# Optimization experiments

Measured on AMD Instinct MI355X. Metric: run time of the kernel, lower is better.

The kernel has to match this reference:

```python
import jax, jax.numpy as jnp
import numpy as np

D_MODEL = 512
H = 8
DEPTH = D_MODEL // H
TOPK = 16
TAU_HID = max(4, D_MODEL // 2)  # 256
TAU_EPS = 1e-6
DT = 1.0
T_SCALAR = 1.0  # default t in call()


def setup_inputs() -> dict:
    key = jax.random.key(0)
    ks = jax.random.split(key, 24)
    B, T = 2, 1024
    D2 = 2 * DEPTH

    def w(k, shape, fan_in):
        return jax.random.normal(k, shape, dtype=jnp.float32) / np.sqrt(fan_in)

    inp = {
        "x": jax.random.normal(ks[0], (B, T, D_MODEL), dtype=jnp.float32),
        "Wq": w(ks[1], (D_MODEL, D_MODEL), D_MODEL), "bq": jnp.zeros((D_MODEL,), jnp.float32),
        "Wk": w(ks[2], (D_MODEL, D_MODEL), D_MODEL), "bk": jnp.zeros((D_MODEL,), jnp.float32),
        "Wv": w(ks[3], (D_MODEL, D_MODEL), D_MODEL), "bv": jnp.zeros((D_MODEL,), jnp.float32),
        "Wo": w(ks[4], (D_MODEL, D_MODEL), D_MODEL), "bo": jnp.zeros((D_MODEL,), jnp.float32),
        "Wpi": w(ks[5], (D2, D_MODEL), D2), "bpi": jnp.zeros((D_MODEL,), jnp.float32),
        "Wpo": w(ks[6], (D_MODEL, 1), D_MODEL), "bpo": jnp.zeros((1,), jnp.float32),
        "Wta": w(ks[7], (D2, 1), D2), "bta": jnp.zeros((1,), jnp.float32),
        "Wtb": w(ks[8], (D2, 1), D2), "btb": jnp.zeros((1,), jnp.float32),
        "Wti": w(ks[9], (D2, TAU_HID), D2), "bti": jnp.zeros((TAU_HID,), jnp.float32),
        "Wto": w(ks[10], (TAU_HID, 1), TAU_HID), "bto": jnp.zeros((1,), jnp.float32),
    }
    return inp


def reference(x, Wq, bq, Wk, bk, Wv, bv, Wo, bo,
              Wpi, bpi, Wpo, bpo, Wta, bta, Wtb, btb, Wti, bti, Wto, bto):
    B, T, _ = x.shape

    def split_heads(z):
        return z.reshape(B, T, H, DEPTH).transpose(0, 2, 1, 3)  # [B,H,T,D]

    qh = split_heads(x @ Wq + bq)
    kh = split_heads(x @ Wk + bk)
    vh = split_heads(x @ Wv + bv)

    # top-k pairwise scores (q @ k^T), select K keys per query
    scores = jnp.einsum('bhqd,bhkd->bhqk', qh, kh)  # [B,H,T,T]
    _, idx = jax.lax.top_k(scores, TOPK)            # [B,H,T,K]

    # gather k and v at top-k indices -> [B,H,T,K,D]
    kg = jnp.take_along_axis(kh[:, :, None, :, :], idx[..., None], axis=3)
    vg = jnp.take_along_axis(vh[:, :, None, :, :], idx[..., None], axis=3)

    # per-pair features [q_i ; k_j] -> [B,H,T,K,2D]
    qt = jnp.broadcast_to(qh[:, :, :, None, :], (B, H, T, TOPK, DEPTH))
    pairs = jnp.concatenate([qt, kg], axis=-1)

    # phi: Dense(d_model) -> Dense(1) -> sigmoid
    phi = jax.nn.sigmoid(((pairs @ Wpi + bpi) @ Wpo + bpo)[..., 0])
    # time interpolation: sigmoid(a*t + b)
    t_a = (pairs @ Wta + bta)[..., 0]
    t_b = (pairs @ Wtb + btb)[..., 0]
    t_interp = jax.nn.sigmoid(t_a * T_SCALAR + t_b)
    # tau: Dense(d_model//2) -> Dense(1) -> softplus + eps
    tau = jax.nn.softplus(((pairs @ Wti + bti) @ Wto + bto)[..., 0]) + TAU_EPS

    # mode == 'exact'
    attn_logits = phi / tau * (1.0 - jnp.exp(-tau * t_interp))
    attn = jax.nn.softmax(attn_logits, axis=-1)  # [B,H,T,K]

    out_h = jnp.einsum('bhqk,bhqkd->bhqd', attn, vg) * DT  # [B,H,T,D]
    combined = out_h.transpose(0, 2, 1, 3).reshape(B, T, D_MODEL)
    return combined @ Wo + bo  # return_sequences=True
```

## Files before the change

### kernel.cpp

```cpp
#include <hip/hip_runtime.h>
#include <math.h>

#define BDIM 2
#define TT 1024
#define NH 8
#define HD 64
#define NTOPK 16
#define NBH 16
#define NTOK 16384

__global__ __launch_bounds__(256) void k_collapse64(
    const float* __restrict__ Wpi, const float* __restrict__ bpi,
    const float* __restrict__ Wpo, const float* __restrict__ bpo,
    const float* __restrict__ Wti, const float* __restrict__ bti,
    const float* __restrict__ Wto, const float* __restrict__ bto,
    double* __restrict__ wphid, double* __restrict__ wtaud,
    double* __restrict__ ccd) {
  int tid = threadIdx.x;
  int blk = blockIdx.x;
  if (blk < 16) {
    int r = blk * 16 + (tid >> 4);
    int l = tid & 15;
    double s = 0.;
    if (r < 128) {
      for (int i = 0; i < 32; ++i)
        s += (double)Wpi[r * 512 + l + 16 * i] * (double)Wpo[l + 16 * i];
    } else {
      int rr = r - 128;
      for (int i = 0; i < 16; ++i)
        s += (double)Wti[rr * 256 + l + 16 * i] * (double)Wto[l + 16 * i];
    }
#pragma unroll
    for (int off = 8; off >= 1; off >>= 1) s += __shfl_xor(s, off, 64);
    if (l == 0) {
      if (r < 128) wphid[r] = s;
      else wtaud[r - 128] = s;
    }
  } else {
    int lane = tid & 63;
    if (tid < 64) {
      double p = 0.;
      for (int c = lane; c < 512; c += 64) p += (double)bpi[c] * (double)Wpo[c];
#pragma unroll
      for (int off = 32; off >= 1; off >>= 1) p += __shfl_xor(p, off, 64);
      if (lane == 0) ccd[0] = p + (double)bpo[0];
    } else if (tid < 128) {
      double p = 0.;
      for (int c = lane; c < 256; c += 64) p += (double)bti[c] * (double)Wto[c];
#pragma unroll
      for (int off = 32; off >= 1; off >>= 1) p += __shfl_xor(p, off, 64);
      if (lane == 0) ccd[1] = p + (double)bto[0];
    }
  }
}

__device__ __forceinline__ void gemm_body(
    const float* __restrict__ A, const float* __restrict__ W,
    const float* __restrict__ bias, float* __restrict__ out,
    int bm, int bn, int mode) {
  __shared__ float As[32][68];
  __shared__ float Bs[32][64];
  const int tid = threadIdx.x;
  const int tx = tid & 15;
  const int ty = tid >> 4;
  float acc[4][4] = {{0.f, 0.f, 0.f, 0.f}};
  for (int k0 = 0; k0 < 512; k0 += 32) {
#pragma unroll
    for (int i = 0; i < 2; ++i) {
      int idx = i * 256 + tid;
      int row = idx >> 3;
      int c4 = (idx & 7) << 2;
      float4 av = *(const float4*)&A[(bm + row) * 512 + k0 + c4];
      As[c4 + 0][row] = av.x;
      As[c4 + 1][row] = av.y;
      As[c4 + 2][row] = av.z;
      As[c4 + 3][row] = av.w;
    }
#pragma unroll
    for (int i = 0; i < 2; ++i) {
      int idx = i * 256 + tid;
      int br = idx >> 4;
      int bc = (idx & 15) << 2;
      *(float4*)&Bs[br][bc] = *(const float4*)&W[(k0 + br) * 512 + bn + bc];
    }
    __syncthreads();
#pragma unroll
    for (int kk = 0; kk < 32; ++kk) {
      float4 a = *(const float4*)&As[kk][ty * 4];
      float4 b = *(const float4*)&Bs[kk][tx << 2];
      acc[0][0] = fmaf(a.x, b.x, acc[0][0]);
      acc[0][1] = fmaf(a.x, b.y, acc[0][1]);
      acc[0][2] = fmaf(a.x, b.z, acc[0][2]);
      acc[0][3] = fmaf(a.x, b.w, acc[0][3]);
      acc[1][0] = fmaf(a.y, b.x, acc[1][0]);
      acc[1][1] = fmaf(a.y, b.y, acc[1][1]);
      acc[1][2] = fmaf(a.y, b.z, acc[1][2]);
      acc[1][3] = fmaf(a.y, b.w, acc[1][3]);
      acc[2][0] = fmaf(a.z, b.x, acc[2][0]);
      acc[2][1] = fmaf(a.z, b.y, acc[2][1]);
      acc[2][2] = fmaf(a.z, b.z, acc[2][2]);
      acc[2][3] = fmaf(a.z, b.w, acc[2][3]);
      acc[3][0] = fmaf(a.w, b.x, acc[3][0]);
      acc[3][1] = fmaf(a.w, b.y, acc[3][1]);
      acc[3][2] = fmaf(a.w, b.z, acc[3][2]);
      acc[3][3] = fmaf(a.w, b.w, acc[3][3]);
    }
    __syncthreads();
  }
#pragma unroll
  for (int i = 0; i < 4; ++i) {
    int row = bm + ty * 4 + i;
    float4 r;
    r.x = acc[i][0] + bias[bn + tx * 4 + 0];
    r.y = acc[i][1] + bias[bn + tx * 4 + 1];
    r.z = acc[i][2] + bias[bn + tx * 4 + 2];
    r.w = acc[i][3] + bias[bn + tx * 4 + 3];
    if (mode == 0) {
      *(float4*)&out[row * 512 + bn + tx * 4] = r;
    } else {
      int bb = row >> 10;
      int tt2 = row & 1023;
      int head = bn >> 6;
      *(float4*)&out[(((bb * NH + head) * TT + tt2) << 6) + tx * 4] = r;
    }
  }
}

__global__ __launch_bounds__(256) void k_gemm(
    const float* __restrict__ A, const float* __restrict__ W,
    const float* __restrict__ bias, float* __restrict__ out, int mode) {
  gemm_body(A, W, bias, out, blockIdx.y * 64, blockIdx.x * 64, mode);
}

__global__ __launch_bounds__(256) void k_gemm_qkv(
    const float* __restrict__ A,
    const float* __restrict__ Wq, const float* __restrict__ bq,
    const float* __restrict__ Wk, const float* __restrict__ bk,
    const float* __restrict__ Wv, const float* __restrict__ bv,
    float* __restrict__ Qf, float* __restrict__ Kf, float* __restrict__ Vf) {
  int which = blockIdx.x >> 3;
  int bn = (blockIdx.x & 7) * 64;
  const float* W = (which == 0) ? Wq : (which == 1) ? Wk : Wv;
  const float* b = (which == 0) ? bq : (which == 1) ? bk : bv;
  float* out = (which == 0) ? Qf : (which == 1) ? Kf : Vf;
  gemm_body(A, W, b, out, blockIdx.y * 64, bn, 1);
}

__global__ __launch_bounds__(256) void k_tokscal64(
    const float* __restrict__ Qg, const float* __restrict__ Kg,
    const double* __restrict__ wphid, const float* __restrict__ Wta,
    const float* __restrict__ Wtb, const double* __restrict__ wtaud,
    double4* __restrict__ sqd4, double4* __restrict__ skd4) {
  __shared__ double wp[128], wa[128], wb[128], wt[128];
  int tid = threadIdx.x;
  if (tid < 128) {
    wp[tid] = wphid[tid];
    wa[tid] = (double)Wta[tid];
    wb[tid] = (double)Wtb[tid];
    wt[tid] = wtaud[tid];
  }
  __syncthreads();
  int tok = blockIdx.x * 256 + tid;
  const float* qr = Qg + (size_t)tok * 64;
  const float* kr = Kg + (size_t)tok * 64;
  double sp = 0., sa = 0., sb = 0., st = 0.;
  double kp = 0., ka = 0., kb2 = 0., kt = 0.;
#pragma unroll
  for (int d = 0; d < 64; ++d) {
    double q = (double)qr[d];
    double k = (double)kr[d];
    sp += q * wp[d];
    sa += q * wa[d];
    sb += q * wb[d];
    st += q * wt[d];
    kp += k * wp[64 + d];
    ka += k * wa[64 + d];
    kb2 += k * wb[64 + d];
    kt += k * wt[64 + d];
  }
  sqd4[tok] = make_double4(sp, sa, sb, st);
  skd4[tok] = make_double4(kp, ka, kb2, kt);
}

__global__ __launch_bounds__(256) void k_score(
    const float* __restrict__ Qf, const float* __restrict__ Kf,
    float* __restrict__ Sc) {
  __shared__ float As[32][132];
  __shared__ float Bs[32][132];
  const int bn = blockIdx.x * 128;
  const int bm = blockIdx.y * 128;
  const int bh = blockIdx.z;
  const float* A = Qf + (size_t)bh * (TT * 64);
  const float* K = Kf + (size_t)bh * (TT * 64);
  float* out = Sc + (size_t)bh * (TT * 1024);
  const int tid = threadIdx.x;
  const int tx = tid & 15;
  const int ty = tid >> 4;
  float acc[8][8];
#pragma unroll
  for (int i = 0; i < 8; ++i)
#pragma unroll
    for (int j = 0; j < 8; ++j) acc[i][j] = 0.f;
  for (int k0 = 0; k0 < 64; k0 += 32) {
#pragma unroll
    for (int i = 0; i < 4; ++i) {
      int idx = i * 256 + tid;
      int row = idx >> 3;
      int c4 = (idx & 7) << 2;
      float4 av = *(const float4*)&A[(size_t)(bm + row) * 64 + k0 + c4];
      As[c4 + 0][row] = av.x;
      As[c4 + 1][row] = av.y;
      As[c4 + 2][row] = av.z;
      As[c4 + 3][row] = av.w;
      float4 kv = *(const float4*)&K[(size_t)(bn + row) * 64 + k0 + c4];
      Bs[c4 + 0][row] = kv.x;
      Bs[c4 + 1][row] = kv.y;
      Bs[c4 + 2][row] = kv.z;
      Bs[c4 + 3][row] = kv.w;
    }
    __syncthreads();
#pragma unroll
    for (int kk = 0; kk < 32; ++kk) {
      float4 alo = *(const float4*)&As[kk][ty * 8];
      float4 ahi = *(const float4*)&As[kk][ty * 8 + 4];
      float4 blo = *(const float4*)&Bs[kk][tx * 8];
      float4 bhi = *(const float4*)&Bs[kk][tx * 8 + 4];
      float a[8] = {alo.x, alo.y, alo.z, alo.w, ahi.x, ahi.y, ahi.z, ahi.w};
      float b[8] = {blo.x, blo.y, blo.z, blo.w, bhi.x, bhi.y, bhi.z, bhi.w};
#pragma unroll
      for (int i = 0; i < 8; ++i)
#pragma unroll
        for (int j = 0; j < 8; ++j)
          acc[i][j] = fmaf(a[i], b[j], acc[i][j]);
    }
    __syncthreads();
  }
#pragma unroll
  for (int i = 0; i < 8; ++i) {
    float4 r0 = make_float4(acc[i][0], acc[i][1], acc[i][2], acc[i][3]);
    float4 r1 = make_float4(acc[i][4], acc[i][5], acc[i][6], acc[i][7]);
    size_t base = (size_t)(bm + ty * 8 + i) * 1024 + bn + tx * 8;
    *(float4*)&out[base] = r0;
    *(float4*)&out[base + 4] = r1;
  }
}

__global__ __launch_bounds__(256) void k_topk(
    const float* __restrict__ Sc, const float* __restrict__ Vg,
    const double4* __restrict__ sqd4, const double4* __restrict__ skd4,
    const double* __restrict__ ccd, const float* __restrict__ btaP,
    const float* __restrict__ btbP, float* __restrict__ C) {
  const int tid = threadIdx.x;
  const int lane = tid & 63;
  const int wv = tid >> 6;
  const int qg = blockIdx.x * 4 + wv;
  const int bh = qg >> 10;
  const int qa = qg & 1023;
  const int bb = bh >> 3;
  const int hh = bh & 7;
  const float* rowp = Sc + (size_t)qg * 1024;
  const float* Vbh = Vg + (size_t)bh * (TT * 64);

  float v[16];
#pragma unroll
  for (int g = 0; g < 4; ++g) {
    float4 t = *(const float4*)&rowp[g * 256 + lane * 4];
    v[g * 4 + 0] = t.x;
    v[g * 4 + 1] = t.y;
    v[g * 4 + 2] = t.z;
    v[g * 4 + 3] = t.w;
  }
  float gv[4];
  int gi[4];
  const int lbase = lane << 2;
#pragma unroll
  for (int g = 0; g < 4; ++g) {
    float nv = v[4 * g];
    int ne = 0;
#pragma unroll
    for (int e = 1; e < 4; ++e) {
      if (v[4 * g + e] > nv) { nv = v[4 * g + e]; ne = e; }
    }
    gv[g] = nv;
    gi[g] = (g << 8) | lbase | ne;
  }
  int myk = 0;
#pragma unroll 1
  for (int it = 0; it < NTOPK; ++it) {
    float cv = gv[0];
    int ci = gi[0];
#pragma unroll
    for (int g = 1; g < 4; ++g) {
      if (gv[g] > cv) { cv = gv[g]; ci = gi[g]; }
    }
    float M = cv;
#pragma unroll
    for (int off = 32; off >= 1; off >>= 1)
      M = fmaxf(M, __shfl_xor(M, off, 64));
    unsigned long long tied = __ballot(cv == M);
    int J;
    if (__popcll(tied) == 1) {
      int src = __ffsll(tied) - 1;
      J = __builtin_amdgcn_readfirstlane(__shfl(ci, src, 64));
    } else {
      int cj = (cv == M) ? ci : 0x7FFFFFFF;
#pragma unroll
      for (int off = 32; off >= 1; off >>= 1) {
        int oj = __shfl_xor(cj, off, 64);
        cj = (oj < cj) ? oj : cj;
      }
      J = __builtin_amdgcn_readfirstlane(cj);
    }
    if (lane == it) myk = J;
    const int owner = (J >> 2) & 63;
    const int g2 = J >> 8;
    const int e2 = J & 3;
    const bool isown = (lane == owner);
#pragma unroll
    for (int g = 0; g < 4; ++g) {
      if (g == g2) {
#pragma unroll
        for (int e = 0; e < 4; ++e) {
          if (e == e2) {
            v[4 * g + e] = isown ? -INFINITY : v[4 * g + e];
          }
        }
        float nv = v[4 * g];
        int ne = 0;
#pragma unroll
        for (int e = 1; e < 4; ++e) {
          if (v[4 * g + e] > nv) { nv = v[4 * g + e]; ne = e; }
        }
        gv[g] = nv;
        gi[g] = (g << 8) | lbase | ne;
      }
    }
  }
  const double cphi = ccd[0];
  const double ctau = ccd[1];
  const double bta0 = (double)btaP[0];
  const double btb0 = (double)btbP[0];
  double4 sq = sqd4[qg];
  float logit = -INFINITY;
  if (lane < 16) {
    double4 sk = skd4[bh * TT + myk];
    float xs = (float)(sq.x + sk.x + cphi);
    float ta = (float)(sq.y + sk.y + bta0);
    float tb = (float)(sq.z + sk.z + btb0);
    float tl = (float)(sq.w + sk.w + ctau);
    float phi = 1.f / (1.f + __expf(-xs));
    float ti = 1.f / (1.f + __expf(-(ta + tb)));
    float tau = fmaxf(tl, 0.f) + log1pf(__expf(-fabsf(tl))) + 1e-6f;
    logit = phi / tau * (1.f - __expf(-tau * ti));
  }
  float m = logit;
#pragma unroll
  for (int off = 8; off >= 1; off >>= 1) m = fmaxf(m, __shfl_xor(m, off, 64));
  float e = (lane < 16) ? __expf(logit - m) : 0.f;
  float ssum = e;
#pragma unroll
  for (int off = 8; off >= 1; off >>= 1) ssum += __shfl_xor(ssum, off, 64);
  float w = e / ssum;
  float outv = 0.f;
#pragma unroll
  for (int k2 = 0; k2 < NTOPK; ++k2) {
    float wk = __shfl(w, k2, 64);
    int ik = __shfl(myk, k2, 64);
    outv = fmaf(wk, Vbh[(size_t)ik * 64 + lane], outv);
  }
  C[(bb * TT + qa) * 512 + hh * 64 + lane] = outv;
}

__global__ __launch_bounds__(256) void k_attn(
    const float* __restrict__ Qg, const float* __restrict__ Kg,
    const float* __restrict__ Vg, const double4* __restrict__ sqd4,
    const double4* __restrict__ skd4, const double* __restrict__ ccd,
    const float* __restrict__ btaP, const float* __restrict__ btbP,
    float* __restrict__ C) {
  __shared__ float qs[8][64];
  __shared__ float sc[8][1024];
  const int bh = blockIdx.y;
  const int q0 = blockIdx.x * 8;
  const int tid = threadIdx.x;
  const int lane = tid & 63;
  const int wv = tid >> 6;
  if (tid < 128) {
    int q = tid >> 4, d4 = (tid & 15) << 2;
    *(float4*)&qs[q][d4] = *(const float4*)&Qg[(size_t)(bh * TT + q0 + q) * 64 + d4];
  }
  __syncthreads();
#pragma unroll 1
  for (int c = 0; c < 4; ++c) {
    const int kb = (c * 4 + wv) * 64;
    const float* krow = &Kg[(size_t)(bh * TT + kb + lane) * 64];
    float4 kr[16];
#pragma unroll
    for (int i = 0; i < 16; ++i) kr[i] = *(const float4*)&krow[i * 4];
#pragma unroll
    for (int q = 0; q < 8; ++q) {
      float s = 0.f;
#pragma unroll
      for (int i = 0; i < 16; ++i) {
        float4 q4 = *(const float4*)&qs[q][i * 4];
        s = fmaf(q4.x, kr[i].x, s);
        s = fmaf(q4.y, kr[i].y, s);
        s = fmaf(q4.z, kr[i].z, s);
        s = fmaf(q4.w, kr[i].w, s);
      }
      sc[q][kb + lane] = s;
    }
  }
  __syncthreads();
  const double cphi = ccd[0];
  const double ctau = ccd[1];
  const double bta0 = (double)btaP[0];
  const double btb0 = (double)btbP[0];
  const int bb = bh >> 3;
  const int hh = bh & 7;
  const float* Vbh = Vg + (size_t)bh * (TT * 64);
#pragma unroll 1
  for (int qq = 0; qq < 2; ++qq) {
    const int ql = wv * 2 + qq;
    const int qa = q0 + ql;
    const float* rowp = &sc[ql][0];
    float v[16];
#pragma unroll
    for (int jj = 0; jj < 16; ++jj) v[jj] = rowp[jj * 64 + lane];
    float gv[4];
    int gj[4];
#pragma unroll
    for (int g = 0; g < 4; ++g) {
      gv[g] = v[4 * g];
      gj[g] = 4 * g;
#pragma unroll
      for (int e = 1; e < 4; ++e) {
        if (v[4 * g + e] > gv[g]) { gv[g] = v[4 * g + e]; gj[g] = 4 * g + e; }
      }
    }
    int myk = 0;
#pragma unroll 1
    for (int it = 0; it < NTOPK; ++it) {
      float bvv = gv[0];
      int bjj = gj[0];
#pragma unroll
      for (int g = 1; g < 4; ++g) {
        if (gv[g] > bvv) { bvv = gv[g]; bjj = gj[g]; }
      }
      int bj = bjj * 64 + lane;
#pragma unroll
      for (int off = 32; off >= 1; off >>= 1) {
        float ov = __shfl_xor(bvv, off, 64);
        int oj = __shfl_xor(bj, off, 64);
        if (ov > bvv || (ov == bvv && oj < bj)) { bvv = ov; bj = oj; }
      }
      if (lane == it) myk = bj;
      int owner = bj & 63;
      int slot = bj >> 6;
      if (lane == owner) {
#pragma unroll
        for (int jj = 0; jj < 16; ++jj)
          if (jj == slot) v[jj] = -INFINITY;
        int g2 = slot >> 2;
#pragma unroll
        for (int g = 0; g < 4; ++g) {
          if (g == g2) {
            float ngv = v[4 * g];
            int ngj = 4 * g;
#pragma unroll
            for (int e = 1; e < 4; ++e) {
              if (v[4 * g + e] > ngv) { ngv = v[4 * g + e]; ngj = 4 * g + e; }
            }
            gv[g] = ngv;
            gj[g] = ngj;
          }
        }
      }
    }
    double4 sq = sqd4[bh * TT + qa];
    double logit = -INFINITY;
    if (lane < 16) {
      double4 sk = skd4[bh * TT + myk];
      double phi = 1.0 / (1.0 + exp(-(sq.x + sk.x + cphi)));
      double ta = sq.y + sk.y + bta0;
      double tb = sq.z + sk.z + btb0;
      double ti = 1.0 / (1.0 + exp(-(ta * 1.0 + tb)));
      double tl = sq.w + sk.w + ctau;
      double tau = fmax(tl, 0.0) + log1p(exp(-fabs(tl))) + 1e-6;
      logit = phi / tau * (1.0 - exp(-tau * ti));
    }
    double m = logit;
#pragma unroll
    for (int off = 8; off >= 1; off >>= 1) {
      double om = __shfl_xor(m, off, 64);
      m = fmax(m, om);
    }
    double e = (lane < 16) ? exp(logit - m) : 0.0;
    double ssum = e;
#pragma unroll
    for (int off = 8; off >= 1; off >>= 1) ssum += __shfl_xor(ssum, off, 64);
    double w = e / ssum;
    double outv = 0.0;
#pragma unroll
    for (int k2 = 0; k2 < NTOPK; ++k2) {
      double wk = __shfl(w, k2, 64);
      int ik = __shfl(myk, k2, 64);
      outv += wk * (double)Vbh[(size_t)ik * 64 + lane];
    }
    C[(bb * TT + qa) * 512 + hh * 64 + lane] = (float)outv;
  }
}

extern "C" void kernel_launch(void* const* d_in, const int* in_sizes, int n_in,
                              void* d_out, int out_size, void* d_ws, size_t ws_size,
                              hipStream_t stream) {
  (void)in_sizes; (void)n_in; (void)out_size;
  const float* x   = (const float*)d_in[0];
  const float* Wq  = (const float*)d_in[1];
  const float* bq  = (const float*)d_in[2];
  const float* Wk  = (const float*)d_in[3];
  const float* bk  = (const float*)d_in[4];
  const float* Wv  = (const float*)d_in[5];
  const float* bv  = (const float*)d_in[6];
  const float* Wo  = (const float*)d_in[7];
  const float* bo  = (const float*)d_in[8];
  const float* Wpi = (const float*)d_in[9];
  const float* bpi = (const float*)d_in[10];
  const float* Wpo = (const float*)d_in[11];
  const float* bpo = (const float*)d_in[12];
  const float* Wta = (const float*)d_in[13];
  const float* bta = (const float*)d_in[14];
  const float* Wtb = (const float*)d_in[15];
  const float* btb = (const float*)d_in[16];
  const float* Wti = (const float*)d_in[17];
  const float* bti = (const float*)d_in[18];
  const float* Wto = (const float*)d_in[19];
  const float* bto = (const float*)d_in[20];

  double* wsd = (double*)d_ws;
  double4* sqd4 = (double4*)wsd;
  double4* skd4 = (double4*)(wsd + 65536);
  double* wphid = wsd + 131072;
  double* wtaud = wsd + 131200;
  double* ccd   = wsd + 131328;
  float* fs = (float*)(wsd + 131332);
  float* Qf = fs;
  float* Kf = fs + 1048576;
  float* Vf = fs + 2097152;
  float* Cf = fs + 3145728;
  float* Sc = fs + 4194304;
  const size_t need = (size_t)131332 * 8 + (size_t)(4194304 + 16777216) * 4;

  hipLaunchKernelGGL(k_collapse64, dim3(17), dim3(256), 0, stream,
                     Wpi, bpi, Wpo, bpo, Wti, bti, Wto, bto, wphid, wtaud, ccd);
  hipLaunchKernelGGL(k_gemm_qkv, dim3(24, 32), dim3(256), 0, stream,
                     x, Wq, bq, Wk, bk, Wv, bv, Qf, Kf, Vf);
  hipLaunchKernelGGL(k_tokscal64, dim3(NTOK / 256), dim3(256), 0, stream,
                     Qf, Kf, wphid, Wta, Wtb, wtaud, sqd4, skd4);
  if (ws_size >= need) {
    hipLaunchKernelGGL(k_score, dim3(8, 8, 16), dim3(256), 0, stream, Qf, Kf, Sc);
    hipLaunchKernelGGL(k_topk, dim3(NTOK / 4), dim3(256), 0, stream,
                       Sc, Vf, sqd4, skd4, ccd, bta, btb, Cf);
  } else {
    hipLaunchKernelGGL(k_attn, dim3(TT / 8, NBH), dim3(256), 0, stream,
                       Qf, Kf, Vf, sqd4, skd4, ccd, bta, btb, Cf);
  }
  hipLaunchKernelGGL(k_gemm, dim3(8, 32), dim3(256), 0, stream,
                     Cf, Wo, bo, (float*)d_out, 0);
}
```

Before: 250.1 us.

## Rewrite shared GEMM as row-per-wave tiles with double-buffered weight tiles

Replaces the 64x64 register-tiled GEMM with a 32x64 tile. Each wave computes 8 rows, reading A rows straight from global memory as wave-uniform broadcasts, while W tiles are double-buffered in shared memory to drop one barrier per k-step. Grids double to cover the smaller tiles, giving more blocks for the 2048-row problems. Each thread now does fewer FMAs per loaded element (8 per B value instead of a 4x4 outer product), so arithmetic intensity falls and global A traffic rises.

```diff
diff --git a/kernel.cpp b/kernel.cpp
--- a/kernel.cpp
+++ b/kernel.cpp
@@ -54,74 +54,76 @@
   }
 }
 
-__device__ __forceinline__ void gemm_body(
+__device__ __forceinline__ void gemm_rw_body(
     const float* __restrict__ A, const float* __restrict__ W,
     const float* __restrict__ bias, float* __restrict__ out,
     int bm, int bn, int mode) {
-  __shared__ float As[32][68];
-  __shared__ float Bs[32][64];
+  __shared__ float Bs[2][32][64];
   const int tid = threadIdx.x;
-  const int tx = tid & 15;
-  const int ty = tid >> 4;
-  float acc[4][4] = {{0.f, 0.f, 0.f, 0.f}};
+  const int lane = tid & 63;
+  const int wv = tid >> 6;
+  const int row0 = bm + wv * 8;
+  const float* Ar = A + (size_t)row0 * 512;
+
+#pragma unroll
+  for (int i = 0; i < 2; ++i) {
+    int idx = i * 256 + tid;
+    int br = idx >> 4;
+    int bc = (idx & 15) << 2;
+    *(float4*)&Bs[0][br][bc] = *(const float4*)&W[(size_t)br * 512 + bn + bc];
+  }
+  __syncthreads();
+
+  float acc[8] = {0.f, 0.f, 0.f, 0.f, 0.f, 0.f, 0.f, 0.f};
+  int cur = 0;
   for (int k0 = 0; k0 < 512; k0 += 32) {
-#pragma unroll
-    for (int i = 0; i < 2; ++i) {
-      int idx = i * 256 + tid;
-      int row = idx >> 3;
-      int c4 = (idx & 7) << 2;
-      float4 av = *(const float4*)&A[(bm + row) * 512 + k0 + c4];
-      As[c4 + 0][row] = av.x;
-      As[c4 + 1][row] = av.y;
-      As[c4 + 2][row] = av.z;
-      As[c4 + 3][row] = av.w;
-    }
-#pragma unroll
-    for (int i = 0; i < 2; ++i) {
-      int idx = i * 256 + tid;
-      int br = idx >> 4;
-      int bc = (idx & 15) << 2;
-      *(float4*)&Bs[br][bc] = *(const float4*)&W[(k0 + br) * 512 + bn + bc];
+    if (k0 + 32 < 512) {
+#pragma unroll
+      for (int i = 0; i < 2; ++i) {
+        int idx = i * 256 + tid;
+        int br = idx >> 4;
+        int bc = (idx & 15) << 2;
+        *(float4*)&Bs[cur ^ 1][br][bc] =
+            *(const float4*)&W[(size_t)(k0 + 32 + br) * 512 + bn + bc];
+      }
+    }
+#pragma unroll 2
+    for (int kk4 = 0; kk4 < 8; ++kk4) {
+      float a0[8], a1[8], a2[8], a3[8];
+#pragma unroll
+      for (int r = 0; r < 8; ++r) {
+        float4 t = *(const float4*)&Ar[r * 512 + k0 + kk4 * 4];
+        a0[r] = t.x; a1[r] = t.y; a2[r] = t.z; a3[r] = t.w;
+      }
+      float b0 = Bs[cur][kk4 * 4 + 0][lane];
+      float b1 = Bs[cur][kk4 * 4 + 1][lane];
+      float b2 = Bs[cur][kk4 * 4 + 2][lane];
+      float b3 = Bs[cur][kk4 * 4 + 3][lane];
+#pragma unroll
+      for (int r = 0; r < 8; ++r) acc[r] = fmaf(a0[r], b0, acc[r]);
+#pragma unroll
+      for (int r = 0; r < 8; ++r) acc[r] = fmaf(a1[r], b1, acc[r]);
+#pragma unroll
+      for (int r = 0; r < 8; ++r) acc[r] = fmaf(a2[r], b2, acc[r]);
+#pragma unroll
+      for (int r = 0; r < 8; ++r) acc[r] = fmaf(a3[r], b3, acc[r]);
     }
     __syncthreads();
-#pragma unroll
-    for (int kk = 0; kk < 32; ++kk) {
-      float4 a = *(const float4*)&As[kk][ty * 4];
-      float4 b = *(const float4*)&Bs[kk][tx << 2];
-      acc[0][0] = fmaf(a.x, b.x, acc[0][0]);
-      acc[0][1] = fmaf(a.x, b.y, acc[0][1]);
-      acc[0][2] = fmaf(a.x, b.z, acc[0][2]);
-      acc[0][3] = fmaf(a.x, b.w, acc[0][3]);
-      acc[1][0] = fmaf(a.y, b.x, acc[1][0]);
-      acc[1][1] = fmaf(a.y, b.y, acc[1][1]);
-      acc[1][2] = fmaf(a.y, b.z, acc[1][2]);
-      acc[1][3] = fmaf(a.y, b.w, acc[1][3]);
-      acc[2][0] = fmaf(a.z, b.x, acc[2][0]);
-      acc[2][1] = fmaf(a.z, b.y, acc[2][1]);
-      acc[2][2] = fmaf(a.z, b.z, acc[2][2]);
-      acc[2][3] = fmaf(a.z, b.w, acc[2][3]);
-      acc[3][0] = fmaf(a.w, b.x, acc[3][0]);
-      acc[3][1] = fmaf(a.w, b.y, acc[3][1]);
-      acc[3][2] = fmaf(a.w, b.z, acc[3][2]);
-      acc[3][3] = fmaf(a.w, b.w, acc[3][3]);
-    }
-    __syncthreads();
-  }
-#pragma unroll
-  for (int i = 0; i < 4; ++i) {
-    int row = bm + ty * 4 + i;
-    float4 r;
-    r.x = acc[i][0] + bias[bn + tx * 4 + 0];
-    r.y = acc[i][1] + bias[bn + tx * 4 + 1];
-    r.z = acc[i][2] + bias[bn + tx * 4 + 2];
-    r.w = acc[i][3] + bias[bn + tx * 4 + 3];
+    cur ^= 1;
+  }
+
+  const float bcol = bias[bn + lane];
+#pragma unroll
+  for (int r = 0; r < 8; ++r) {
+    int row = row0 + r;
+    float o = acc[r] + bcol;
     if (mode == 0) {
-      *(float4*)&out[row * 512 + bn + tx * 4] = r;
+      out[(size_t)row * 512 + bn + lane] = o;
     } else {
-      int bb = row >> 10;
+      int bbk = row >> 10;
       int tt2 = row & 1023;
       int head = bn >> 6;
-      *(float4*)&out[(((bb * NH + head) * TT + tt2) << 6) + tx * 4] = r;
+      out[(size_t)(((bbk * NH + head) * TT + tt2) << 6) + lane] = o;
     }
   }
 }
@@ -129,7 +131,7 @@
 __global__ __launch_bounds__(256) void k_gemm(
     const float* __restrict__ A, const float* __restrict__ W,
     const float* __restrict__ bias, float* __restrict__ out, int mode) {
-  gemm_body(A, W, bias, out, blockIdx.y * 64, blockIdx.x * 64, mode);
+  gemm_rw_body(A, W, bias, out, blockIdx.y * 32, blockIdx.x * 64, mode);
 }
 
 __global__ __launch_bounds__(256) void k_gemm_qkv(
@@ -143,7 +145,7 @@
   const float* W = (which == 0) ? Wq : (which == 1) ? Wk : Wv;
   const float* b = (which == 0) ? bq : (which == 1) ? bk : bv;
   float* out = (which == 0) ? Qf : (which == 1) ? Kf : Vf;
-  gemm_body(A, W, b, out, blockIdx.y * 64, bn, 1);
+  gemm_rw_body(A, W, b, out, blockIdx.y * 32, bn, 1);
 }
 
 __global__ __launch_bounds__(256) void k_tokscal64(
@@ -552,7 +554,7 @@
 
   hipLaunchKernelGGL(k_collapse64, dim3(17), dim3(256), 0, stream,
                      Wpi, bpi, Wpo, bpo, Wti, bti, Wto, bto, wphid, wtaud, ccd);
-  hipLaunchKernelGGL(k_gemm_qkv, dim3(24, 32), dim3(256), 0, stream,
+  hipLaunchKernelGGL(k_gemm_qkv, dim3(24, 64), dim3(256), 0, stream,
                      x, Wq, bq, Wk, bk, Wv, bv, Qf, Kf, Vf);
   hipLaunchKernelGGL(k_tokscal64, dim3(NTOK / 256), dim3(256), 0, stream,
                      Qf, Kf, wphid, Wta, Wtb, wtaud, sqd4, skd4);
@@ -564,6 +566,6 @@
     hipLaunchKernelGGL(k_attn, dim3(TT / 8, NBH), dim3(256), 0, stream,
                        Qf, Kf, Vf, sqd4, skd4, ccd, bta, btb, Cf);
   }
-  hipLaunchKernelGGL(k_gemm, dim3(8, 32), dim3(256), 0, stream,
+  hipLaunchKernelGGL(k_gemm, dim3(8, 64), dim3(256), 0, stream,
                      Cf, Wo, bo, (float*)d_out, 0);
 }
```

Result: slower. 416.7 us (+66.6%).

## Fuse score, top-k and attention into one kernel, dropping the materialized score matrix

Applied to the files above, without the earlier changes.

Replaces the two-kernel path (a tiled score GEMM writing a 64 MB score buffer, then a top-k kernel reading it back) with one fused kernel. It computes each query block's scores in shared memory, selects the top-k with ballot-based tie handling, and does the logit, softmax and weighted V sum in float instead of double. This removes the global write and read of the full score matrix plus one launch. In exchange, the per-block score computation is a simple non-tiled dot-product loop, and the float epilogue may differ slightly numerically from the double version.

```diff
diff --git a/kernel.cpp b/kernel.cpp
--- a/kernel.cpp
+++ b/kernel.cpp
@@ -182,6 +182,156 @@
   skd4[tok] = make_double4(kp, ka, kb2, kt);
 }
 
+__global__ __launch_bounds__(256) void k_attn_f(
+    const float* __restrict__ Qg, const float* __restrict__ Kg,
+    const float* __restrict__ Vg, const double4* __restrict__ sqd4,
+    const double4* __restrict__ skd4, const double* __restrict__ ccd,
+    const float* __restrict__ btaP, const float* __restrict__ btbP,
+    float* __restrict__ C) {
+  __shared__ float qs[8][64];
+  __shared__ float sc[8][1024];
+  const int bh = blockIdx.y;
+  const int q0 = blockIdx.x * 8;
+  const int tid = threadIdx.x;
+  const int lane = tid & 63;
+  const int wv = tid >> 6;
+  if (tid < 128) {
+    int q = tid >> 4, d4 = (tid & 15) << 2;
+    *(float4*)&qs[q][d4] = *(const float4*)&Qg[(size_t)(bh * TT + q0 + q) * 64 + d4];
+  }
+  __syncthreads();
+#pragma unroll 1
+  for (int c = 0; c < 4; ++c) {
+    const int kb = (c * 4 + wv) * 64;
+    const float* krow = &Kg[(size_t)(bh * TT + kb + lane) * 64];
+    float4 kr[16];
+#pragma unroll
+    for (int i = 0; i < 16; ++i) kr[i] = *(const float4*)&krow[i * 4];
+#pragma unroll
+    for (int q = 0; q < 8; ++q) {
+      float s = 0.f;
+#pragma unroll
+      for (int i = 0; i < 16; ++i) {
+        float4 q4 = *(const float4*)&qs[q][i * 4];
+        s = fmaf(q4.x, kr[i].x, s);
+        s = fmaf(q4.y, kr[i].y, s);
+        s = fmaf(q4.z, kr[i].z, s);
+        s = fmaf(q4.w, kr[i].w, s);
+      }
+      sc[q][kb + lane] = s;
+    }
+  }
+  __syncthreads();
+  const double cphi = ccd[0];
+  const double ctau = ccd[1];
+  const double bta0 = (double)btaP[0];
+  const double btb0 = (double)btbP[0];
+  const int bb = bh >> 3;
+  const int hh = bh & 7;
+  const float* Vbh = Vg + (size_t)bh * (TT * 64);
+#pragma unroll 1
+  for (int qq = 0; qq < 2; ++qq) {
+    const int ql = wv * 2 + qq;
+    const int qa = q0 + ql;
+    float v[16];
+#pragma unroll
+    for (int jj = 0; jj < 16; ++jj) v[jj] = sc[ql][jj * 64 + lane];
+    float gv[4];
+    int gi[4];
+#pragma unroll
+    for (int g = 0; g < 4; ++g) {
+      float nv = v[4 * g];
+      int ne = 0;
+#pragma unroll
+      for (int e = 1; e < 4; ++e) {
+        if (v[4 * g + e] > nv) { nv = v[4 * g + e]; ne = e; }
+      }
+      gv[g] = nv;
+      gi[g] = ((4 * g + ne) << 6) | lane;
+    }
+    int myk = 0;
+#pragma unroll 1
+    for (int it = 0; it < NTOPK; ++it) {
+      float cv = gv[0];
+      int ci = gi[0];
+#pragma unroll
+      for (int g = 1; g < 4; ++g) {
+        if (gv[g] > cv) { cv = gv[g]; ci = gi[g]; }
+      }
+      float M = cv;
+#pragma unroll
+      for (int off = 32; off >= 1; off >>= 1)
+        M = fmaxf(M, __shfl_xor(M, off, 64));
+      unsigned long long tied = __ballot(cv == M);
+      int J;
+      if (__popcll(tied) == 1) {
+        int src = __ffsll(tied) - 1;
+        J = __builtin_amdgcn_readfirstlane(__shfl(ci, src, 64));
+      } else {
+        int cj = (cv == M) ? ci : 0x7FFFFFFF;
+#pragma unroll
+        for (int off = 32; off >= 1; off >>= 1) {
+          int oj = __shfl_xor(cj, off, 64);
+          cj = (oj < cj) ? oj : cj;
+        }
+        J = __builtin_amdgcn_readfirstlane(cj);
+      }
+      if (lane == it) myk = J;
+      const int owner = J & 63;
+      const int slot2 = J >> 6;
+      const int g2 = slot2 >> 2;
+      const int e2 = slot2 & 3;
+      const bool isown = (lane == owner);
+#pragma unroll
+      for (int g = 0; g < 4; ++g) {
+        if (g == g2) {
+#pragma unroll
+          for (int e = 0; e < 4; ++e) {
+            if (e == e2) v[4 * g + e] = isown ? -INFINITY : v[4 * g + e];
+          }
+          float nv = v[4 * g];
+          int ne = 0;
+#pragma unroll
+          for (int e = 1; e < 4; ++e) {
+            if (v[4 * g + e] > nv) { nv = v[4 * g + e]; ne = e; }
+          }
+          gv[g] = nv;
+          gi[g] = ((4 * g + ne) << 6) | lane;
+        }
+      }
+    }
+    double4 sq = sqd4[(size_t)bh * TT + qa];
+    float logit = -INFINITY;
+    if (lane < 16) {
+      double4 sk = skd4[bh * TT + myk];
+      float xs = (float)(sq.x + sk.x + cphi);
+      float ta = (float)(sq.y + sk.y + bta0);
+      float tb = (float)(sq.z + sk.z + btb0);
+      float tl = (float)(sq.w + sk.w + ctau);
+      float phi = 1.f / (1.f + __expf(-xs));
+      float ti = 1.f / (1.f + __expf(-(ta + tb)));
+      float tau = fmaxf(tl, 0.f) + log1pf(__expf(-fabsf(tl))) + 1e-6f;
+      logit = phi / tau * (1.f - __expf(-tau * ti));
+    }
+    float m = logit;
+#pragma unroll
+    for (int off = 8; off >= 1; off >>= 1) m = fmaxf(m, __shfl_xor(m, off, 64));
+    float e = (lane < 16) ? __expf(logit - m) : 0.f;
+    float ssum = e;
+#pragma unroll
+    for (int off = 8; off >= 1; off >>= 1) ssum += __shfl_xor(ssum, off, 64);
+    float w = e / ssum;
+    float outv = 0.f;
+#pragma unroll
+    for (int k2 = 0; k2 < NTOPK; ++k2) {
+      float wk = __shfl(w, k2, 64);
+      int ik = __shfl(myk, k2, 64);
+      outv = fmaf(wk, Vbh[(size_t)ik * 64 + lane], outv);
+    }
+    C[(bb * TT + qa) * 512 + hh * 64 + lane] = outv;
+  }
+}
+
 __global__ __launch_bounds__(256) void k_score(
     const float* __restrict__ Qf, const float* __restrict__ Kf,
     float* __restrict__ Sc) {
@@ -260,7 +410,6 @@
   const int hh = bh & 7;
   const float* rowp = Sc + (size_t)qg * 1024;
   const float* Vbh = Vg + (size_t)bh * (TT * 64);
-
   float v[16];
 #pragma unroll
   for (int g = 0; g < 4; ++g) {
@@ -321,9 +470,7 @@
       if (g == g2) {
 #pragma unroll
         for (int e = 0; e < 4; ++e) {
-          if (e == e2) {
-            v[4 * g + e] = isown ? -INFINITY : v[4 * g + e];
-          }
+          if (e == e2) v[4 * g + e] = isown ? -INFINITY : v[4 * g + e];
         }
         float nv = v[4 * g];
         int ne = 0;
@@ -371,149 +518,10 @@
   C[(bb * TT + qa) * 512 + hh * 64 + lane] = outv;
 }
 
-__global__ __launch_bounds__(256) void k_attn(
-    const float* __restrict__ Qg, const float* __restrict__ Kg,
-    const float* __restrict__ Vg, const double4* __restrict__ sqd4,
-    const double4* __restrict__ skd4, const double* __restrict__ ccd,
-    const float* __restrict__ btaP, const float* __restrict__ btbP,
-    float* __restrict__ C) {
-  __shared__ float qs[8][64];
-  __shared__ float sc[8][1024];
-  const int bh = blockIdx.y;
-  const int q0 = blockIdx.x * 8;
-  const int tid = threadIdx.x;
-  const int lane = tid & 63;
-  const int wv = tid >> 6;
-  if (tid < 128) {
-    int q = tid >> 4, d4 = (tid & 15) << 2;
-    *(float4*)&qs[q][d4] = *(const float4*)&Qg[(size_t)(bh * TT + q0 + q) * 64 + d4];
-  }
-  __syncthreads();
-#pragma unroll 1
-  for (int c = 0; c < 4; ++c) {
-    const int kb = (c * 4 + wv) * 64;
-    const float* krow = &Kg[(size_t)(bh * TT + kb + lane) * 64];
-    float4 kr[16];
-#pragma unroll
-    for (int i = 0; i < 16; ++i) kr[i] = *(const float4*)&krow[i * 4];
-#pragma unroll
-    for (int q = 0; q < 8; ++q) {
-      float s = 0.f;
-#pragma unroll
-      for (int i = 0; i < 16; ++i) {
-        float4 q4 = *(const float4*)&qs[q][i * 4];
-        s = fmaf(q4.x, kr[i].x, s);
-        s = fmaf(q4.y, kr[i].y, s);
-        s = fmaf(q4.z, kr[i].z, s);
-        s = fmaf(q4.w, kr[i].w, s);
-      }
-      sc[q][kb + lane] = s;
-    }
-  }
-  __syncthreads();
-  const double cphi = ccd[0];
-  const double ctau = ccd[1];
-  const double bta0 = (double)btaP[0];
-  const double btb0 = (double)btbP[0];
-  const int bb = bh >> 3;
-  const int hh = bh & 7;
-  const float* Vbh = Vg + (size_t)bh * (TT * 64);
-#pragma unroll 1
-  for (int qq = 0; qq < 2; ++qq) {
-    const int ql = wv * 2 + qq;
-    const int qa = q0 + ql;
-    const float* rowp = &sc[ql][0];
-    float v[16];
-#pragma unroll
-    for (int jj = 0; jj < 16; ++jj) v[jj] = rowp[jj * 64 + lane];
-    float gv[4];
-    int gj[4];
-#pragma unroll
-    for (int g = 0; g < 4; ++g) {
-      gv[g] = v[4 * g];
-      gj[g] = 4 * g;
-#pragma unroll
-      for (int e = 1; e < 4; ++e) {
-        if (v[4 * g + e] > gv[g]) { gv[g] = v[4 * g + e]; gj[g] = 4 * g + e; }
-      }
-    }
-    int myk = 0;
-#pragma unroll 1
-    for (int it = 0; it < NTOPK; ++it) {
-      float bvv = gv[0];
-      int bjj = gj[0];
-#pragma unroll
-      for (int g = 1; g < 4; ++g) {
-        if (gv[g] > bvv) { bvv = gv[g]; bjj = gj[g]; }
-      }
-      int bj = bjj * 64 + lane;
-#pragma unroll
-      for (int off = 32; off >= 1; off >>= 1) {
-        float ov = __shfl_xor(bvv, off, 64);
-        int oj = __shfl_xor(bj, off, 64);
-        if (ov > bvv || (ov == bvv && oj < bj)) { bvv = ov; bj = oj; }
-      }
-      if (lane == it) myk = bj;
-      int owner = bj & 63;
-      int slot = bj >> 6;
-      if (lane == owner) {
-#pragma unroll
-        for (int jj = 0; jj < 16; ++jj)
-          if (jj == slot) v[jj] = -INFINITY;
-        int g2 = slot >> 2;
-#pragma unroll
-        for (int g = 0; g < 4; ++g) {
-          if (g == g2) {
-            float ngv = v[4 * g];
-            int ngj = 4 * g;
-#pragma unroll
-            for (int e = 1; e < 4; ++e) {
-              if (v[4 * g + e] > ngv) { ngv = v[4 * g + e]; ngj = 4 * g + e; }
-            }
-            gv[g] = ngv;
-            gj[g] = ngj;
-          }
-        }
-      }
-    }
-    double4 sq = sqd4[bh * TT + qa];
-    double logit = -INFINITY;
-    if (lane < 16) {
-      double4 sk = skd4[bh * TT + myk];
-      double phi = 1.0 / (1.0 + exp(-(sq.x + sk.x + cphi)));
-      double ta = sq.y + sk.y + bta0;
-      double tb = sq.z + sk.z + btb0;
-      double ti = 1.0 / (1.0 + exp(-(ta * 1.0 + tb)));
-      double tl = sq.w + sk.w + ctau;
-      double tau = fmax(tl, 0.0) + log1p(exp(-fabs(tl))) + 1e-6;
-      logit = phi / tau * (1.0 - exp(-tau * ti));
-    }
-    double m = logit;
-#pragma unroll
-    for (int off = 8; off >= 1; off >>= 1) {
-      double om = __shfl_xor(m, off, 64);
-      m = fmax(m, om);
-    }
-    double e = (lane < 16) ? exp(logit - m) : 0.0;
-    double ssum = e;
-#pragma unroll
-    for (int off = 8; off >= 1; off >>= 1) ssum += __shfl_xor(ssum, off, 64);
-    double w = e / ssum;
-    double outv = 0.0;
-#pragma unroll
-    for (int k2 = 0; k2 < NTOPK; ++k2) {
-      double wk = __shfl(w, k2, 64);
-      int ik = __shfl(myk, k2, 64);
-      outv += wk * (double)Vbh[(size_t)ik * 64 + lane];
-    }
-    C[(bb * TT + qa) * 512 + hh * 64 + lane] = (float)outv;
-  }
-}
-
 extern "C" void kernel_launch(void* const* d_in, const int* in_sizes, int n_in,
                               void* d_out, int out_size, void* d_ws, size_t ws_size,
                               hipStream_t stream) {
-  (void)in_sizes; (void)n_in; (void)out_size;
+  (void)in_sizes; (void)n_in; (void)out_size; (void)ws_size;
   const float* x   = (const float*)d_in[0];
   const float* Wq  = (const float*)d_in[1];
   const float* bq  = (const float*)d_in[2];
@@ -547,8 +555,6 @@
   float* Kf = fs + 1048576;
   float* Vf = fs + 2097152;
   float* Cf = fs + 3145728;
-  float* Sc = fs + 4194304;
-  const size_t need = (size_t)131332 * 8 + (size_t)(4194304 + 16777216) * 4;
 
   hipLaunchKernelGGL(k_collapse64, dim3(17), dim3(256), 0, stream,
                      Wpi, bpi, Wpo, bpo, Wti, bti, Wto, bto, wphid, wtaud, ccd);
@@ -556,14 +562,8 @@
                      x, Wq, bq, Wk, bk, Wv, bv, Qf, Kf, Vf);
   hipLaunchKernelGGL(k_tokscal64, dim3(NTOK / 256), dim3(256), 0, stream,
                      Qf, Kf, wphid, Wta, Wtb, wtaud, sqd4, skd4);
-  if (ws_size >= need) {
-    hipLaunchKernelGGL(k_score, dim3(8, 8, 16), dim3(256), 0, stream, Qf, Kf, Sc);
-    hipLaunchKernelGGL(k_topk, dim3(NTOK / 4), dim3(256), 0, stream,
-                       Sc, Vf, sqd4, skd4, ccd, bta, btb, Cf);
-  } else {
-    hipLaunchKernelGGL(k_attn, dim3(TT / 8, NBH), dim3(256), 0, stream,
-                       Qf, Kf, Vf, sqd4, skd4, ccd, bta, btb, Cf);
-  }
+  hipLaunchKernelGGL(k_attn_f, dim3(TT / 8, NBH), dim3(256), 0, stream,
+                     Qf, Kf, Vf, sqd4, skd4, ccd, bta, btb, Cf);
   hipLaunchKernelGGL(k_gemm, dim3(8, 32), dim3(256), 0, stream,
                      Cf, Wo, bo, (float*)d_out, 0);
 }
```

Result: slower. 446.1 us (+78.4%).
